# Performance work log

Measured on AMD Instinct MI355X. Metric: run time of the kernel, lower is better.

Reference implementation:

```python
import jax, jax.numpy as jnp
import numpy as np

EMBED_DIM = 64  # scale factor dim (matches head dim)


def setup_inputs() -> dict:
    key0 = jax.random.key(0)
    kq, kk, kv = jax.random.split(key0, 3)
    shape = (2, 16, 2048, 64)  # [B, H, S, D]
    return {
        "query": jax.random.normal(kq, shape, dtype=jnp.float32),
        "key": jax.random.normal(kk, shape, dtype=jnp.float32),
        "value": jax.random.normal(kv, shape, dtype=jnp.float32),
    }


def reference(query, key, value):
    # qk = Q K^T / sqrt(embed_dim); softmax over last dim; @ V
    inv_scale = jnp.sqrt(jnp.asarray(EMBED_DIM, dtype=query.dtype))
    scores = jnp.einsum("bhqd,bhkd->bhqk", query, key) / inv_scale
    probs = jax.nn.softmax(scores, axis=-1)
    # dropout_p=0.0 -> identity (eval semantics)
    return jnp.einsum("bhqk,bhkd->bhqd", probs, value)
```

## Files before the change

### kernel.cpp

```cpp
#include <hip/hip_runtime.h>
#include <hip/hip_bf16.h>

#define S_LEN 2048
#define DDIM  64
#define NT    (S_LEN / 64)
#define SCALE  0.125f
#define SCALE2 0.18033688f
#define NELEM  4194304
#define NQROW  65536

typedef __attribute__((ext_vector_type(8))) short short8;
typedef __attribute__((ext_vector_type(4))) short short4v;
typedef __attribute__((ext_vector_type(4))) float floatx4;

__device__ __forceinline__ short f2bf(float f) {
    union { float f; unsigned u; } v; v.f = f;
    return (short)((v.u + 0x7fffu + ((v.u >> 16) & 1u)) >> 16);
}

__device__ __forceinline__ float fexp2(float x) {
#if __has_builtin(__builtin_amdgcn_exp2f)
    return __builtin_amdgcn_exp2f(x);
#else
    return exp2f(x);
#endif
}

__device__ __forceinline__ void dma16(const void* g, void* l) {
    __builtin_amdgcn_global_load_lds(
        (const __attribute__((address_space(1))) void*)g,
        (__attribute__((address_space(3))) void*)l, 16, 0, 0);
}

__global__ __launch_bounds__(256) void prep_kv(const float* __restrict__ K,
                                               const float* __restrict__ V,
                                               short* __restrict__ Kb,
                                               short* __restrict__ Vt) {
    __shared__ short T[64 * 68];
    const int bh = blockIdx.x & 31;
    const int st = blockIdx.x >> 5;
    const int t  = threadIdx.x;
    const size_t tile_off = (size_t)bh * (S_LEN * DDIM) + (size_t)st * (64 * DDIM);

    {
        const float* src = K + tile_off + t * 16;
        short* dst = Kb + tile_off + t * 16;
        #pragma unroll
        for (int h = 0; h < 2; ++h) {
            float4 a = *(const float4*)(src + h * 8);
            float4 b = *(const float4*)(src + h * 8 + 4);
            short8 o;
            o[0]=f2bf(a.x); o[1]=f2bf(a.y); o[2]=f2bf(a.z); o[3]=f2bf(a.w);
            o[4]=f2bf(b.x); o[5]=f2bf(b.y); o[6]=f2bf(b.z); o[7]=f2bf(b.w);
            *(short8*)(dst + h * 8) = o;
        }
    }

    const float* src = V + tile_off;
    const int skey = t >> 2, scol = (t & 3) * 4;
    #pragma unroll
    for (int i = 0; i < 4; ++i) {
        const int c = scol + i * 16;
        float4 v = *(const float4*)(src + (size_t)skey * 64 + c);
        short4v o; o[0]=f2bf(v.x); o[1]=f2bf(v.y); o[2]=f2bf(v.z); o[3]=f2bf(v.w);
        *(short4v*)&T[skey * 68 + c] = o;
    }
    __syncthreads();
    const int d = t >> 2, cb = (t & 3) * 16;
    short8 o0, o1;
    #pragma unroll
    for (int j = 0; j < 8; ++j) {
        o0[j] = T[(cb + j) * 68 + d];
        o1[j] = T[(cb + 8 + j) * 68 + d];
    }
    short* dst = Vt + (size_t)bh * (DDIM * S_LEN) + (size_t)d * S_LEN + st * 64 + cb;
    *(short8*)dst       = o0;
    *(short8*)(dst + 8) = o1;
}

template <int NSPLIT>
__global__ __launch_bounds__(256) void attn_sm(
    const float* __restrict__ Q, const short* __restrict__ Kb,
    const short* __restrict__ Vt, float* __restrict__ O,
    float* __restrict__ numer, float* __restrict__ denom)
{
    __shared__ short Ks[2][64 * 64];
    __shared__ short Vs[2][64 * 64];
    __shared__ short Pl[4][32 * 72];

    constexpr int NIT = NT / NSPLIT;

    const int tid  = threadIdx.x;
    const int wave = tid >> 6;
    const int lane = tid & 63;
    const int l16  = lane & 15;
    const int quad = lane >> 4;
    const int x7   = l16 & 7;

    const int bh = blockIdx.x & 31;
    const int rest = blockIdx.x >> 5;
    const int qt = rest & 15;
    const int ks = rest >> 4;
    const size_t base = (size_t)bh * (S_LEN * DDIM);

    const int ci0 = tid,        r0 = ci0 >> 3, c0 = (ci0 & 7) ^ (r0 & 7);
    const int ci1 = 256 + tid,  r1 = ci1 >> 3, c1 = (ci1 & 7) ^ (r1 & 7);
    const size_t koff = (size_t)ks * NIT * (64 * 64);
    const size_t voff = (size_t)ks * NIT * 64;
    const short* pK0 = Kb + base + koff + r0 * 64 + c0 * 8;
    const short* pK1 = Kb + base + koff + r1 * 64 + c1 * 8;
    const short* pV0 = Vt + base + voff + (size_t)r0 * S_LEN + c0 * 8;
    const short* pV1 = Vt + base + voff + (size_t)r1 * S_LEN + c1 * 8;

    dma16(pK0, &Ks[0][ci0 * 8]);
    dma16(pK1, &Ks[0][ci1 * 8]);
    dma16(pV0, &Vs[0][ci0 * 8]);
    dma16(pV1, &Vs[0][ci1 * 8]);

    short8 qf[2][2];
    #pragma unroll
    for (int mt = 0; mt < 2; ++mt) {
        const float* qp = Q + base + (size_t)(qt * 128 + wave * 32 + mt * 16 + l16) * 64 + quad * 8;
        #pragma unroll
        for (int kt = 0; kt < 2; ++kt) {
            float4 a = *(const float4*)(qp + kt * 32);
            float4 b = *(const float4*)(qp + kt * 32 + 4);
            short* d = (short*)&qf[mt][kt];
            d[0]=f2bf(a.x*SCALE2); d[1]=f2bf(a.y*SCALE2); d[2]=f2bf(a.z*SCALE2); d[3]=f2bf(a.w*SCALE2);
            d[4]=f2bf(b.x*SCALE2); d[5]=f2bf(b.y*SCALE2); d[6]=f2bf(b.z*SCALE2); d[7]=f2bf(b.w*SCALE2);
        }
    }

    floatx4 oacc[2][4];
    float rs[2][4];
    #pragma unroll
    for (int mt = 0; mt < 2; ++mt) {
        #pragma unroll
        for (int dt = 0; dt < 4; ++dt) oacc[mt][dt] = (floatx4){0.f,0.f,0.f,0.f};
        #pragma unroll
        for (int r = 0; r < 4; ++r) rs[mt][r] = 0.f;
    }

    short* Pw = &Pl[wave][0];

    for (int kb = 0; kb < NIT; ++kb) {
        const int cur = kb & 1;
        __syncthreads();

        if (kb + 1 < NIT) {
            const int nxt = cur ^ 1;
            const int ok = (kb + 1) * (64 * 64), ov = (kb + 1) * 64;
            dma16(pK0 + ok, &Ks[nxt][ci0 * 8]);
            dma16(pK1 + ok, &Ks[nxt][ci1 * 8]);
            dma16(pV0 + ov, &Vs[nxt][ci0 * 8]);
            dma16(pV1 + ov, &Vs[nxt][ci1 * 8]);
        }

        const short* ks_ = Ks[cur];
        floatx4 sc[2][4];
        #pragma unroll
        for (int nt = 0; nt < 4; ++nt) {
            floatx4 a0 = (floatx4){0.f,0.f,0.f,0.f};
            floatx4 a1 = (floatx4){0.f,0.f,0.f,0.f};
            #pragma unroll
            for (int kt = 0; kt < 2; ++kt) {
                const int csw = (kt * 4 + quad) ^ x7;
                short8 kf = *(const short8*)&ks_[(nt * 16 + l16) * 64 + csw * 8];
                a0 = __builtin_amdgcn_mfma_f32_16x16x32_bf16(qf[0][kt], kf, a0, 0, 0, 0);
                a1 = __builtin_amdgcn_mfma_f32_16x16x32_bf16(qf[1][kt], kf, a1, 0, 0, 0);
            }
            sc[0][nt] = a0; sc[1][nt] = a1;
        }

        #pragma unroll
        for (int mt = 0; mt < 2; ++mt) {
            #pragma unroll
            for (int r = 0; r < 4; ++r) {
                const int prow = (mt * 16 + quad * 4 + r) * 72;
                #pragma unroll
                for (int nt = 0; nt < 4; ++nt) {
                    float p = fexp2(sc[mt][nt][r]);
                    rs[mt][r] += p;
                    Pw[prow + nt * 16 + l16] = f2bf(p);
                }
            }
        }

        const short* vs = Vs[cur];
        #pragma unroll
        for (int kt = 0; kt < 2; ++kt) {
            short8 pf0 = *(const short8*)&Pw[(l16)      * 72 + kt * 32 + quad * 8];
            short8 pf1 = *(const short8*)&Pw[(16 + l16) * 72 + kt * 32 + quad * 8];
            const int csw = (kt * 4 + quad) ^ x7;
            #pragma unroll
            for (int dt = 0; dt < 4; ++dt) {
                short8 vf = *(const short8*)&vs[(dt * 16 + l16) * 64 + csw * 8];
                oacc[0][dt] = __builtin_amdgcn_mfma_f32_16x16x32_bf16(pf0, vf, oacc[0][dt], 0, 0, 0);
                oacc[1][dt] = __builtin_amdgcn_mfma_f32_16x16x32_bf16(pf1, vf, oacc[1][dt], 0, 0, 0);
            }
        }
    }

    #pragma unroll
    for (int mt = 0; mt < 2; ++mt) {
        #pragma unroll
        for (int r = 0; r < 4; ++r) {
            float s = rs[mt][r];
            s += __shfl_xor(s, 1, 64);
            s += __shfl_xor(s, 2, 64);
            s += __shfl_xor(s, 4, 64);
            s += __shfl_xor(s, 8, 64);
            const int row = qt * 128 + wave * 32 + mt * 16 + quad * 4 + r;
            if (NSPLIT == 1) {
                const float inv = 1.0f / s;
                float* op = O + base + (size_t)row * 64 + l16;
                #pragma unroll
                for (int dt = 0; dt < 4; ++dt)
                    op[dt * 16] = oacc[mt][dt][r] * inv;
            } else {
                float* np = numer + (size_t)ks * NELEM + base + (size_t)row * 64 + l16;
                #pragma unroll
                for (int dt = 0; dt < 4; ++dt)
                    np[dt * 16] = oacc[mt][dt][r];
                if (l16 == 0)
                    denom[(size_t)ks * NQROW + bh * S_LEN + row] = s;
            }
        }
    }
}

__global__ __launch_bounds__(256) void combine2(const float* __restrict__ numer,
                                                const float* __restrict__ denom,
                                                float* __restrict__ O) {
    const size_t i = ((size_t)blockIdx.x * 256 + threadIdx.x) * 4;
    const size_t q = i >> 6;
    const float inv = 1.0f / (denom[q] + denom[NQROW + q]);
    float4 n0 = *(const float4*)(numer + i);
    float4 n1 = *(const float4*)(numer + NELEM + i);
    float4 o;
    o.x = (n0.x + n1.x) * inv;
    o.y = (n0.y + n1.y) * inv;
    o.z = (n0.z + n1.z) * inv;
    o.w = (n0.w + n1.w) * inv;
    *(float4*)(O + i) = o;
}

#define BQ    64
#define BKEY  64
#define KPAD  72

__global__ __launch_bounds__(256) void attn_kernel(
    const float* __restrict__ Q, const float* __restrict__ K,
    const float* __restrict__ V, float* __restrict__ O)
{
    __shared__ short Ksh[BKEY * KPAD];
    __shared__ short Vtt[DDIM * KPAD];
    __shared__ short Pls[4][16 * KPAD];

    const int tid  = threadIdx.x;
    const int wave = tid >> 6;
    const int lane = tid & 63;
    const int l16  = lane & 15;
    const int quad = lane >> 4;

    const int bh = blockIdx.x & 31;
    const int qt = blockIdx.x >> 5;
    const size_t base = (size_t)bh * S_LEN * DDIM;

    const int qrow = qt * BQ + wave * 16 + l16;
    short8 qf[2];
    {
        const float* qp = Q + base + (size_t)qrow * DDIM + quad * 8;
        #pragma unroll
        for (int kt = 0; kt < 2; ++kt) {
            float4 a = *(const float4*)(qp + kt * 32);
            float4 b = *(const float4*)(qp + kt * 32 + 4);
            short* d = (short*)&qf[kt];
            d[0]=f2bf(a.x*SCALE); d[1]=f2bf(a.y*SCALE); d[2]=f2bf(a.z*SCALE); d[3]=f2bf(a.w*SCALE);
            d[4]=f2bf(b.x*SCALE); d[5]=f2bf(b.y*SCALE); d[6]=f2bf(b.z*SCALE); d[7]=f2bf(b.w*SCALE);
        }
    }

    float m_i[4], l_i[4];
    floatx4 oacc[4];
    #pragma unroll
    for (int r = 0; r < 4; ++r) { m_i[r] = -3.0e38f; l_i[r] = 0.f; }
    #pragma unroll
    for (int dt = 0; dt < 4; ++dt) oacc[dt] = (floatx4){0.f, 0.f, 0.f, 0.f};

    const int skey = tid >> 2;
    const int scol = (tid & 3) * 4;

    for (int kb = 0; kb < S_LEN / BKEY; ++kb) {
        const float* Kg = K + base + (size_t)kb * BKEY * DDIM + (size_t)skey * DDIM;
        const float* Vg = V + base + (size_t)kb * BKEY * DDIM + (size_t)skey * DDIM;
        #pragma unroll
        for (int i = 0; i < 4; ++i) {
            const int c = scol + i * 16;
            float4 kv = *(const float4*)(Kg + c);
            short* kd = &Ksh[skey * KPAD + c];
            kd[0]=f2bf(kv.x); kd[1]=f2bf(kv.y); kd[2]=f2bf(kv.z); kd[3]=f2bf(kv.w);
            float4 vv = *(const float4*)(Vg + c);
            Vtt[(c+0)*KPAD + skey] = f2bf(vv.x);
            Vtt[(c+1)*KPAD + skey] = f2bf(vv.y);
            Vtt[(c+2)*KPAD + skey] = f2bf(vv.z);
            Vtt[(c+3)*KPAD + skey] = f2bf(vv.w);
        }
        __syncthreads();

        floatx4 sc[4];
        #pragma unroll
        for (int nt = 0; nt < 4; ++nt) {
            floatx4 acc = (floatx4){0.f, 0.f, 0.f, 0.f};
            #pragma unroll
            for (int kt = 0; kt < 2; ++kt) {
                short8 kf = *(const short8*)&Ksh[(nt*16 + l16) * KPAD + kt*32 + quad*8];
                acc = __builtin_amdgcn_mfma_f32_16x16x32_bf16(qf[kt], kf, acc, 0, 0, 0);
            }
            sc[nt] = acc;
        }

        short* Pw = &Pls[wave][0];
        #pragma unroll
        for (int r = 0; r < 4; ++r) {
            float mx = fmaxf(fmaxf(sc[0][r], sc[1][r]), fmaxf(sc[2][r], sc[3][r]));
            #pragma unroll
            for (int off = 1; off < 16; off <<= 1)
                mx = fmaxf(mx, __shfl_xor(mx, off, 64));
            const float mnew  = fmaxf(m_i[r], mx);
            const float alpha = __expf(m_i[r] - mnew);
            m_i[r] = mnew;
            float rsum = 0.f;
            #pragma unroll
            for (int nt = 0; nt < 4; ++nt) {
                float p = __expf(sc[nt][r] - mnew);
                rsum += p;
                Pw[(quad*4 + r) * KPAD + nt*16 + l16] = f2bf(p);
            }
            #pragma unroll
            for (int off = 1; off < 16; off <<= 1)
                rsum += __shfl_xor(rsum, off, 64);
            l_i[r] = l_i[r] * alpha + rsum;
            oacc[0][r] *= alpha; oacc[1][r] *= alpha;
            oacc[2][r] *= alpha; oacc[3][r] *= alpha;
        }

        #pragma unroll
        for (int kt = 0; kt < 2; ++kt) {
            short8 pf = *(const short8*)&Pw[l16 * KPAD + kt*32 + quad*8];
            #pragma unroll
            for (int dt = 0; dt < 4; ++dt) {
                short8 vf = *(const short8*)&Vtt[(dt*16 + l16) * KPAD + kt*32 + quad*8];
                oacc[dt] = __builtin_amdgcn_mfma_f32_16x16x32_bf16(pf, vf, oacc[dt], 0, 0, 0);
            }
        }
        __syncthreads();
    }

    #pragma unroll
    for (int r = 0; r < 4; ++r) {
        const float inv = 1.0f / l_i[r];
        const int row = qt * BQ + wave * 16 + quad * 4 + r;
        float* op = O + base + (size_t)row * DDIM + l16;
        #pragma unroll
        for (int dt = 0; dt < 4; ++dt)
            op[dt * 16] = oacc[dt][r] * inv;
    }
}

extern "C" void kernel_launch(void* const* d_in, const int* in_sizes, int n_in,
                              void* d_out, int out_size, void* d_ws, size_t ws_size,
                              hipStream_t stream) {
    const float* Q = (const float*)d_in[0];
    const float* K = (const float*)d_in[1];
    const float* V = (const float*)d_in[2];
    float* O = (float*)d_out;

    const size_t prep_bytes = (size_t)NELEM * 2 * 2;
    const size_t split_bytes = prep_bytes + (size_t)2 * NELEM * 4
                             + (size_t)2 * NQROW * 4;

    if (ws_size >= split_bytes) {
        short* Kb  = (short*)d_ws;
        short* Vtp = (short*)d_ws + NELEM;
        float* num = (float*)((char*)d_ws + prep_bytes);
        float* den = num + (size_t)2 * NELEM;
        prep_kv<<<dim3(1024), dim3(256), 0, stream>>>(K, V, Kb, Vtp);
        attn_sm<2><<<dim3(1024), dim3(256), 0, stream>>>(Q, Kb, Vtp, nullptr, num, den);
        combine2<<<dim3(NELEM / 1024), dim3(256), 0, stream>>>(num, den, O);
    } else if (ws_size >= prep_bytes) {
        short* Kb  = (short*)d_ws;
        short* Vtp = (short*)d_ws + NELEM;
        prep_kv<<<dim3(1024), dim3(256), 0, stream>>>(K, V, Kb, Vtp);
        attn_sm<1><<<dim3(512), dim3(256), 0, stream>>>(Q, Kb, Vtp, O, nullptr, nullptr);
    } else {
        attn_kernel<<<dim3(1024), dim3(256), 0, stream>>>(Q, K, V, O);
    }
}
```

Baseline: 162.3 us.

## Compute transposed S tile so P writes become vectorized swizzled stores

Swaps the MFMA operands in the QK^T step so each lane holds four consecutive key scores for one query row. P can then be written to LDS as 4-element vector stores into an XOR-swizzled 64-wide buffer instead of scalar stores into a padded 72-wide one. Row sums collapse to one accumulator per tile, reduced with two cross-quad shuffles, and are redistributed with __shfl for the final normalization. This lowers LDS store count and shuffle work but adds shuffle traffic in the epilogue, and it depends on the swizzle matching the read pattern.

```diff
diff --git a/kernel.cpp b/kernel.cpp
--- a/kernel.cpp
+++ b/kernel.cpp
@@ -86,7 +86,7 @@
 {
     __shared__ short Ks[2][64 * 64];
     __shared__ short Vs[2][64 * 64];
-    __shared__ short Pl[4][32 * 72];
+    __shared__ short Pl[4][32 * 64];
 
     constexpr int NIT = NT / NSPLIT;
 
@@ -119,26 +119,25 @@
 
     short8 qf[2][2];
     #pragma unroll
-    for (int mt = 0; mt < 2; ++mt) {
-        const float* qp = Q + base + (size_t)(qt * 128 + wave * 32 + mt * 16 + l16) * 64 + quad * 8;
+    for (int nq = 0; nq < 2; ++nq) {
+        const float* qp = Q + base + (size_t)(qt * 128 + wave * 32 + nq * 16 + l16) * 64 + quad * 8;
         #pragma unroll
         for (int kt = 0; kt < 2; ++kt) {
             float4 a = *(const float4*)(qp + kt * 32);
             float4 b = *(const float4*)(qp + kt * 32 + 4);
-            short* d = (short*)&qf[mt][kt];
+            short* d = (short*)&qf[nq][kt];
             d[0]=f2bf(a.x*SCALE2); d[1]=f2bf(a.y*SCALE2); d[2]=f2bf(a.z*SCALE2); d[3]=f2bf(a.w*SCALE2);
             d[4]=f2bf(b.x*SCALE2); d[5]=f2bf(b.y*SCALE2); d[6]=f2bf(b.z*SCALE2); d[7]=f2bf(b.w*SCALE2);
         }
     }
 
     floatx4 oacc[2][4];
-    float rs[2][4];
+    float rs[2];
     #pragma unroll
     for (int mt = 0; mt < 2; ++mt) {
         #pragma unroll
         for (int dt = 0; dt < 4; ++dt) oacc[mt][dt] = (floatx4){0.f,0.f,0.f,0.f};
-        #pragma unroll
-        for (int r = 0; r < 4; ++r) rs[mt][r] = 0.f;
+        rs[mt] = 0.f;
     }
 
     short* Pw = &Pl[wave][0];
@@ -159,39 +158,42 @@
         const short* ks_ = Ks[cur];
         floatx4 sc[2][4];
         #pragma unroll
-        for (int nt = 0; nt < 4; ++nt) {
+        for (int mk = 0; mk < 4; ++mk) {
             floatx4 a0 = (floatx4){0.f,0.f,0.f,0.f};
             floatx4 a1 = (floatx4){0.f,0.f,0.f,0.f};
             #pragma unroll
             for (int kt = 0; kt < 2; ++kt) {
                 const int csw = (kt * 4 + quad) ^ x7;
-                short8 kf = *(const short8*)&ks_[(nt * 16 + l16) * 64 + csw * 8];
-                a0 = __builtin_amdgcn_mfma_f32_16x16x32_bf16(qf[0][kt], kf, a0, 0, 0, 0);
-                a1 = __builtin_amdgcn_mfma_f32_16x16x32_bf16(qf[1][kt], kf, a1, 0, 0, 0);
-            }
-            sc[0][nt] = a0; sc[1][nt] = a1;
-        }
-
-        #pragma unroll
-        for (int mt = 0; mt < 2; ++mt) {
-            #pragma unroll
-            for (int r = 0; r < 4; ++r) {
-                const int prow = (mt * 16 + quad * 4 + r) * 72;
-                #pragma unroll
-                for (int nt = 0; nt < 4; ++nt) {
-                    float p = fexp2(sc[mt][nt][r]);
-                    rs[mt][r] += p;
-                    Pw[prow + nt * 16 + l16] = f2bf(p);
-                }
+                short8 kf = *(const short8*)&ks_[(mk * 16 + l16) * 64 + csw * 8];
+                a0 = __builtin_amdgcn_mfma_f32_16x16x32_bf16(kf, qf[0][kt], a0, 0, 0, 0);
+                a1 = __builtin_amdgcn_mfma_f32_16x16x32_bf16(kf, qf[1][kt], a1, 0, 0, 0);
+            }
+            sc[0][mk] = a0; sc[1][mk] = a1;
+        }
+
+        #pragma unroll
+        for (int nq = 0; nq < 2; ++nq) {
+            const int prow = (nq * 16 + l16) * 64;
+            #pragma unroll
+            for (int mk = 0; mk < 4; ++mk) {
+                float p0 = fexp2(sc[nq][mk][0]);
+                float p1 = fexp2(sc[nq][mk][1]);
+                float p2 = fexp2(sc[nq][mk][2]);
+                float p3 = fexp2(sc[nq][mk][3]);
+                rs[nq] += (p0 + p1) + (p2 + p3);
+                short4v pv;
+                pv[0]=f2bf(p0); pv[1]=f2bf(p1); pv[2]=f2bf(p2); pv[3]=f2bf(p3);
+                const int c8 = (mk * 4 + quad) ^ (2 * x7);
+                *(short4v*)&Pw[prow + c8 * 4] = pv;
             }
         }
 
         const short* vs = Vs[cur];
         #pragma unroll
         for (int kt = 0; kt < 2; ++kt) {
-            short8 pf0 = *(const short8*)&Pw[(l16)      * 72 + kt * 32 + quad * 8];
-            short8 pf1 = *(const short8*)&Pw[(16 + l16) * 72 + kt * 32 + quad * 8];
             const int csw = (kt * 4 + quad) ^ x7;
+            short8 pf0 = *(const short8*)&Pw[(l16)      * 64 + csw * 8];
+            short8 pf1 = *(const short8*)&Pw[(16 + l16) * 64 + csw * 8];
             #pragma unroll
             for (int dt = 0; dt < 4; ++dt) {
                 short8 vf = *(const short8*)&vs[(dt * 16 + l16) * 64 + csw * 8];
@@ -201,31 +203,39 @@
         }
     }
 
+    float inv[2];
+    #pragma unroll
+    for (int nq = 0; nq < 2; ++nq) {
+        float s = rs[nq];
+        s += __shfl_xor(s, 16, 64);
+        s += __shfl_xor(s, 32, 64);
+        if (NSPLIT == 2) {
+            if (quad == 0)
+                denom[(size_t)ks * NQROW + bh * S_LEN + qt * 128 + wave * 32 + nq * 16 + l16] = s;
+        }
+        inv[nq] = 1.0f / s;
+    }
+
     #pragma unroll
     for (int mt = 0; mt < 2; ++mt) {
+        const float dv = (NSPLIT == 1) ? __shfl(inv[mt], quad * 4, 64) : 0.f;
         #pragma unroll
         for (int r = 0; r < 4; ++r) {
-            float s = rs[mt][r];
-            s += __shfl_xor(s, 1, 64);
-            s += __shfl_xor(s, 2, 64);
-            s += __shfl_xor(s, 4, 64);
-            s += __shfl_xor(s, 8, 64);
             const int row = qt * 128 + wave * 32 + mt * 16 + quad * 4 + r;
             if (NSPLIT == 1) {
-                const float inv = 1.0f / s;
+                const float d_r = __shfl(inv[mt], quad * 4 + r, 64);
                 float* op = O + base + (size_t)row * 64 + l16;
                 #pragma unroll
                 for (int dt = 0; dt < 4; ++dt)
-                    op[dt * 16] = oacc[mt][dt][r] * inv;
+                    op[dt * 16] = oacc[mt][dt][r] * d_r;
             } else {
                 float* np = numer + (size_t)ks * NELEM + base + (size_t)row * 64 + l16;
                 #pragma unroll
                 for (int dt = 0; dt < 4; ++dt)
                     np[dt * 16] = oacc[mt][dt][r];
-                if (l16 == 0)
-                    denom[(size_t)ks * NQROW + bh * S_LEN + row] = s;
-            }
-        }
+            }
+        }
+        (void)dv;
     }
 }
 
```

Result: faster. 158.0 us (-2.6%).
